# Kernel optimization log

Hardware: AMD Instinct MI355X
Metric: run time of the kernel (lower is better)

The kernel has to match this reference:

```python
import jax, jax.numpy as jnp
import numpy as np

B, L, D = 4, 2048, 1024
H, HD = 16, 64
SCALE = 1.0 / np.sqrt(H).astype(np.float32)  # NOTE: source divides by sqrt(head_num), not sqrt(head_dim)
NEG = -10000000.0


def setup_inputs() -> dict:
    key = jax.random.key(0)
    ks = jax.random.split(key, 7)
    s = 1.0 / np.sqrt(D).astype(np.float32)
    return {
        "X": jax.random.normal(ks[0], (B, L, D), dtype=jnp.float32),
        "Wq": jax.random.normal(ks[1], (D, D), dtype=jnp.float32) * s,
        "bq": jnp.zeros((D,), dtype=jnp.float32),
        "Wk": jax.random.normal(ks[2], (D, D), dtype=jnp.float32) * s,
        "bk": jnp.zeros((D,), dtype=jnp.float32),
        "Wv": jax.random.normal(ks[3], (D, D), dtype=jnp.float32) * s,
        "bv": jnp.zeros((D,), dtype=jnp.float32),
    }


def _split_heads(x):
    # [B, L, D] -> [B, H, L, HD]
    return x.reshape(B, L, H, HD).transpose(0, 2, 1, 3)


def reference(X, Wq, bq, Wk, bk, Wv, bv):
    Q = _split_heads(X @ Wq.T + bq)
    K = _split_heads(X @ Wk.T + bk)
    V = _split_heads(X @ Wv.T + bv)
    logits = jnp.einsum('bhld,bhmd->bhlm', Q, K) * SCALE
    # causal mask: strictly-upper-triangular entries get a large negative additive bias
    mask = jnp.triu(jnp.full((L, L), NEG, dtype=logits.dtype), k=1)
    logits = logits + mask[None, None, :, :]
    w = jax.nn.softmax(logits, axis=-1)
    out = jnp.einsum('bhlm,bhmd->bhld', w, V)
    # combine heads: [B, H, L, HD] -> [B, L, D]
    return out.transpose(0, 2, 1, 3).reshape(B, L, H * HD)
```

## Files before the change

### kernel.cpp

```cpp
#include <hip/hip_runtime.h>
#include <hip/hip_bf16.h>

#define L_SEQ   2048
#define DMODEL  1024
#define NH      16
#define HD      64
#define MROWS   8192
#define QSC     0.360673760222f
#define NEG2    -2.0e7f

typedef float  f32x4 __attribute__((ext_vector_type(4)));
typedef short  s16x8 __attribute__((ext_vector_type(8)));

__device__ __forceinline__ unsigned short f2bf(float f) {
    union { float f; unsigned u; } v; v.f = f;
    unsigned r = (v.u + 0x7FFFu + ((v.u >> 16) & 1u)) >> 16;
    return (unsigned short)r;
}

__device__ __forceinline__ float fexp2(float x) {
#if __has_builtin(__builtin_amdgcn_exp2f)
    return __builtin_amdgcn_exp2f(x);
#else
    return __expf(x * 0.6931471805599453f);
#endif
}

__device__ __forceinline__ unsigned pk2(float a, float b) {
    union { float f; unsigned u; } ua, ub; ua.f = a; ub.f = b;
    return __builtin_amdgcn_perm(ub.u, ua.u, 0x07060302u);
}

__device__ __forceinline__ void gl_lds16(const void* g, void* l) {
    __builtin_amdgcn_global_load_lds(
        (const __attribute__((address_space(1))) unsigned int*)g,
        (__attribute__((address_space(3))) unsigned int*)l, 16, 0, 0);
}

__global__ __launch_bounds__(256) void cvt_all(const float* __restrict__ X,
                                               const float* __restrict__ W0,
                                               const float* __restrict__ W1,
                                               const float* __restrict__ W2,
                                               unsigned short* __restrict__ Xb,
                                               unsigned short* __restrict__ Wb) {
    const int bx = blockIdx.x, tid = threadIdx.x;
    const float* src; unsigned short* dst; int i;
    if (bx < 8192) {
        src = X; dst = Xb; i = bx * 256 + tid;
    } else {
        int r = bx - 8192; const int wsel = r >> 10; r &= 1023;
        src = (wsel == 0) ? W0 : (wsel == 1) ? W1 : W2;
        dst = Wb + (size_t)wsel * (DMODEL * DMODEL);
        i = r * 256 + tid;
    }
    float4 v = ((const float4*)src)[i];
    ushort4 o;
    o.x = f2bf(v.x); o.y = f2bf(v.y); o.z = f2bf(v.z); o.w = f2bf(v.w);
    ((ushort4*)dst)[i] = o;
}

__global__ __launch_bounds__(256, 2) void qkv_gemm(
        const unsigned short* __restrict__ Xb,
        const unsigned short* __restrict__ Wb,
        const float* __restrict__ bq, const float* __restrict__ bk_,
        const float* __restrict__ bv,
        unsigned short* __restrict__ Yb) {
    __shared__ unsigned short As[128 * 32];
    __shared__ unsigned short Bs[128 * 32];

    const int tid = threadIdx.x;
    const int w = tid >> 6, l = tid & 63, q = l >> 4, t = l & 15;
    const int mw = w >> 1, nw = w & 1;
    const int z = blockIdx.z;
    const int rowM0 = blockIdx.x * 128;
    const int colN0 = blockIdx.y * 128;

    const unsigned short* W = Wb + (size_t)z * (DMODEL * DMODEL);
    unsigned short* Y = Yb + (size_t)z * ((size_t)MROWS * DMODEL);
    const float* bias = (z == 0) ? bq : (z == 1) ? bk_ : bv;
    const float osc = (z == 0) ? QSC : 1.0f;

    f32x4 acc[4][4] = {};

    const int srow = l >> 2;
    const int scol = (l & 3) * 8;

    for (int k0 = 0; k0 < DMODEL; k0 += 32) {
        #pragma unroll
        for (int r = 0; r < 2; ++r) {
            const int row = w * 32 + r * 16;
            gl_lds16(Xb + (size_t)(rowM0 + row + srow) * DMODEL + k0 + scol, As + row * 32);
            gl_lds16(W  + (size_t)(colN0 + row + srow) * DMODEL + k0 + scol, Bs + row * 32);
        }
        __syncthreads();
        s16x8 a[4], b[4];
        #pragma unroll
        for (int i = 0; i < 4; ++i) {
            a[i] = *(const s16x8*)&As[(mw * 64 + i * 16 + t) * 32 + q * 8];
            b[i] = *(const s16x8*)&Bs[(nw * 64 + i * 16 + t) * 32 + q * 8];
        }
        #pragma unroll
        for (int in = 0; in < 4; ++in)
            #pragma unroll
            for (int jm = 0; jm < 4; ++jm)
                acc[in][jm] = __builtin_amdgcn_mfma_f32_16x16x32_bf16(b[in], a[jm], acc[in][jm], 0, 0, 0);
        __syncthreads();
    }

    #pragma unroll
    for (int in = 0; in < 4; ++in) {
        const int ncol = colN0 + nw * 64 + in * 16 + q * 4;
        const float4 b4 = *(const float4*)&bias[ncol];
        #pragma unroll
        for (int jm = 0; jm < 4; ++jm) {
            const int mrow = rowM0 + mw * 64 + jm * 16 + t;
            unsigned lo = ((unsigned)f2bf((acc[in][jm][0] + b4.x) * osc)) |
                          ((unsigned)f2bf((acc[in][jm][1] + b4.y) * osc) << 16);
            unsigned hi = ((unsigned)f2bf((acc[in][jm][2] + b4.z) * osc)) |
                          ((unsigned)f2bf((acc[in][jm][3] + b4.w) * osc) << 16);
            uint2 o; o.x = lo; o.y = hi;
            *(uint2*)&Y[(size_t)mrow * DMODEL + ncol] = o;
        }
    }
}

#define SKV 72

__global__ __launch_bounds__(256, 4) void attn_fwd(
        const unsigned short* __restrict__ Qb,
        const unsigned short* __restrict__ Kb,
        const unsigned short* __restrict__ Vb,
        float* __restrict__ out) {
    __shared__ __align__(16) unsigned short Ks[2][64 * 64];
    __shared__ __align__(16) unsigned short Vt[2][64 * SKV];

    const int tid = threadIdx.x;
    const int w = tid >> 6, l = tid & 63, q = l >> 4, t = l & 15;

    const int lin = blockIdx.y * gridDim.x + blockIdx.x;
    const int xcd = lin & 7;
    const int slot = lin >> 3;
    const int bh = ((slot >> 4) << 3) | xcd;
    const int pairx = slot & 15;

    const int b = bh >> 4, h = bh & 15;
    const size_t base = ((size_t)b * L_SEQ) * DMODEL + h * HD;

    const int d8 = tid >> 5, jp = tid & 31;
    const int vslot = ((jp >> 4) << 5) | (((jp >> 1) & 3) << 3) | (((jp >> 3) & 1) << 2) | ((jp & 1) << 1);
    const int krow_in = l >> 3;
    const int kchunk_g = (l & 7) ^ krow_in;

    int kaddr[4][2];
    #pragma unroll
    for (int nt = 0; nt < 4; ++nt)
        #pragma unroll
        for (int ks = 0; ks < 2; ++ks)
            kaddr[nt][ks] = (nt * 16 + t) * 64 + (((ks * 4 + q) ^ (t & 7)) * 8);

    s16x8 vone;
    #pragma unroll
    for (int i = 0; i < 8; ++i) vone[i] = (short)0x3F80;

    auto stageK = [&](int jbase, unsigned short* dst) {
        #pragma unroll
        for (int r = 0; r < 2; ++r) {
            const int rb = r * 4 + w;
            gl_lds16(Kb + base + (size_t)(jbase + rb * 8 + krow_in) * DMODEL + kchunk_g * 8,
                     dst + rb * 512);
        }
    };
    auto stageV = [&](int jbase, unsigned short* dst) {
        const unsigned short* vp = Vb + base + (size_t)(jbase + 2 * jp) * DMODEL + d8 * 8;
        uint4 v0 = *(const uint4*)vp;
        uint4 v1 = *(const uint4*)(vp + DMODEL);
        const unsigned* u0 = (const unsigned*)&v0;
        const unsigned* u1 = (const unsigned*)&v1;
        #pragma unroll
        for (int i = 0; i < 4; ++i) {
            *(unsigned*)&dst[(d8 * 8 + 2 * i)     * SKV + vslot] = __builtin_amdgcn_perm(u1[i], u0[i], 0x05040100u);
            *(unsigned*)&dst[(d8 * 8 + 2 * i + 1) * SKV + vslot] = __builtin_amdgcn_perm(u1[i], u0[i], 0x07060302u);
        }
    };

    for (int pass = 0; pass < 2; ++pass) {
        const int qt = pass ? (31 - pairx) : pairx;
        const int qbase = qt * 64;

        s16x8 bq[2];
        {
            const unsigned short* qp = Qb + base + (size_t)(qbase + w * 16 + t) * DMODEL + q * 8;
            bq[0] = *(const s16x8*)(qp);
            bq[1] = *(const s16x8*)(qp + 32);
        }

        float m_i = -__builtin_inff();
        f32x4 accO[4] = {};
        f32x4 accL = {};

        auto loadS = [&](const unsigned short* KsBuf, f32x4* stt) {
            #pragma unroll
            for (int nt = 0; nt < 4; ++nt) {
                f32x4 zz = {};
                #pragma unroll
                for (int ks = 0; ks < 2; ++ks) {
                    s16x8 ak = *(const s16x8*)&KsBuf[kaddr[nt][ks]];
                    zz = __builtin_amdgcn_mfma_f32_16x16x32_bf16(ak, bq[ks], zz, 0, 0, 0);
                }
                stt[nt] = zz;
            }
        };
        auto maskS = [&](f32x4* stt) {
            const int rhs = w * 16 + t;
            #pragma unroll
            for (int nt = 0; nt < 4; ++nt)
                #pragma unroll
                for (int r = 0; r < 4; ++r)
                    if (nt * 16 + q * 4 + r > rhs) stt[nt][r] += NEG2;
        };
        auto rescale = [&](float m_new) {
            const float alpha = fexp2(m_i - m_new);
            m_i = m_new;
            float ar[4];
            #pragma unroll
            for (int r = 0; r < 4; ++r) ar[r] = __shfl(alpha, q * 4 + r, 64);
            #pragma unroll
            for (int nt = 0; nt < 4; ++nt)
                #pragma unroll
                for (int r = 0; r < 4; ++r) accO[nt][r] *= ar[r];
            #pragma unroll
            for (int r = 0; r < 4; ++r) accL[r] *= ar[r];
        };
        auto pvAcc = [&](const f32x4* stt, float m_new, const unsigned short* VtBuf) {
            union { unsigned u[8]; s16x8 h[2]; } P;
            #pragma unroll
            for (int nt = 0; nt < 4; ++nt) {
                float p0 = fexp2(stt[nt][0] - m_new);
                float p1 = fexp2(stt[nt][1] - m_new);
                float p2 = fexp2(stt[nt][2] - m_new);
                float p3 = fexp2(stt[nt][3] - m_new);
                P.u[2 * nt]     = pk2(p0, p1);
                P.u[2 * nt + 1] = pk2(p2, p3);
            }
            #pragma unroll
            for (int ks = 0; ks < 2; ++ks) {
                #pragma unroll
                for (int nt = 0; nt < 4; ++nt) {
                    s16x8 vb = *(const s16x8*)&VtBuf[(nt * 16 + t) * SKV + ks * 32 + q * 8];
                    accO[nt] = __builtin_amdgcn_mfma_f32_16x16x32_bf16(P.h[ks], vb, accO[nt], 0, 0, 0);
                }
                accL = __builtin_amdgcn_mfma_f32_16x16x32_bf16(P.h[ks], vone, accL, 0, 0, 0);
            }
        };

        int jt = 0;
        for (; jt + 1 <= qt; jt += 2) {
            __syncthreads();
            stageK(jt * 64, Ks[0]); stageK(jt * 64 + 64, Ks[1]);
            stageV(jt * 64, Vt[0]); stageV(jt * 64 + 64, Vt[1]);
            __syncthreads();

            f32x4 s0[4], s1[4];
            loadS(Ks[0], s0);
            loadS(Ks[1], s1);
            if (jt + 1 == qt) maskS(s1);

            float mx = s0[0][0];
            #pragma unroll
            for (int nt = 0; nt < 4; ++nt)
                #pragma unroll
                for (int r = 0; r < 4; ++r) { mx = fmaxf(mx, s0[nt][r]); mx = fmaxf(mx, s1[nt][r]); }
            mx = fmaxf(mx, __shfl_xor(mx, 16, 64));
            mx = fmaxf(mx, __shfl_xor(mx, 32, 64));
            const float m_new = fmaxf(m_i, mx);

            rescale(m_new);
            pvAcc(s0, m_new, Vt[0]);
            pvAcc(s1, m_new, Vt[1]);
        }
        if (jt == qt) {
            __syncthreads();
            stageK(qbase, Ks[0]);
            stageV(qbase, Vt[0]);
            __syncthreads();

            f32x4 s0[4];
            loadS(Ks[0], s0);
            maskS(s0);

            float mx = s0[0][0];
            #pragma unroll
            for (int nt = 0; nt < 4; ++nt)
                #pragma unroll
                for (int r = 0; r < 4; ++r) mx = fmaxf(mx, s0[nt][r]);
            mx = fmaxf(mx, __shfl_xor(mx, 16, 64));
            mx = fmaxf(mx, __shfl_xor(mx, 32, 64));
            const float m_new = fmaxf(m_i, mx);

            rescale(m_new);
            pvAcc(s0, m_new, Vt[0]);
        }

        float inv_r[4];
        #pragma unroll
        for (int r = 0; r < 4; ++r) inv_r[r] = 1.0f / accL[r];
        #pragma unroll
        for (int nt = 0; nt < 4; ++nt) {
            #pragma unroll
            for (int r = 0; r < 4; ++r) {
                const int row = qbase + w * 16 + q * 4 + r;
                out[((size_t)(b * L_SEQ + row)) * DMODEL + h * HD + nt * 16 + t] =
                    accO[nt][r] * inv_r[r];
            }
        }
    }
}

extern "C" void kernel_launch(void* const* d_in, const int* in_sizes, int n_in,
                              void* d_out, int out_size, void* d_ws, size_t ws_size,
                              hipStream_t stream) {
    const float* X  = (const float*)d_in[0];
    const float* Wq = (const float*)d_in[1];
    const float* bq = (const float*)d_in[2];
    const float* Wk = (const float*)d_in[3];
    const float* bk = (const float*)d_in[4];
    const float* Wv = (const float*)d_in[5];
    const float* bv = (const float*)d_in[6];
    float* out = (float*)d_out;

    unsigned short* Xb = (unsigned short*)d_ws;
    unsigned short* Wb = Xb + (size_t)MROWS * DMODEL;
    unsigned short* Yb = Wb + (size_t)3 * DMODEL * DMODEL;

    cvt_all<<<8192 + 3 * 1024, 256, 0, stream>>>(X, Wq, Wk, Wv, Xb, Wb);

    qkv_gemm<<<dim3(64, 8, 3), 256, 0, stream>>>(Xb, Wb, bq, bk, bv, Yb);

    const size_t hs = (size_t)MROWS * DMODEL;
    attn_fwd<<<dim3(16, 64), 256, 0, stream>>>(Yb, Yb + hs, Yb + 2 * hs, out);
}
```

Measured before the change: 229.7 us.

## Write QKV in head-major layout and widen GEMM K-tile with swizzled LDS

The QKV GEMM epilogue now writes Q/K/V in [B,H,L,HD] order, so the attention kernel reads contiguous 128-byte rows per head instead of strided rows across the full model dimension. The GEMM K-step doubles to 64 with an XOR-swizzled shared-memory layout, which halves the barrier count and aims to reduce LDS bank conflicts. This costs more LDS per block, which may reduce occupancy, and the epilogue's global stores are now scattered across heads.

```diff
diff --git a/kernel.cpp b/kernel.cpp
--- a/kernel.cpp
+++ b/kernel.cpp
@@ -65,8 +65,8 @@
         const float* __restrict__ bq, const float* __restrict__ bk_,
         const float* __restrict__ bv,
         unsigned short* __restrict__ Yb) {
-    __shared__ unsigned short As[128 * 32];
-    __shared__ unsigned short Bs[128 * 32];
+    __shared__ unsigned short As[128 * 64];
+    __shared__ unsigned short Bs[128 * 64];
 
     const int tid = threadIdx.x;
     const int w = tid >> 6, l = tid & 63, q = l >> 4, t = l & 15;
@@ -82,44 +82,54 @@
 
     f32x4 acc[4][4] = {};
 
-    const int srow = l >> 2;
-    const int scol = (l & 3) * 8;
-
-    for (int k0 = 0; k0 < DMODEL; k0 += 32) {
-        #pragma unroll
-        for (int r = 0; r < 2; ++r) {
-            const int row = w * 32 + r * 16;
-            gl_lds16(Xb + (size_t)(rowM0 + row + srow) * DMODEL + k0 + scol, As + row * 32);
-            gl_lds16(W  + (size_t)(colN0 + row + srow) * DMODEL + k0 + scol, Bs + row * 32);
+    const int srow8 = l >> 3;
+    const int sch_g = ((l & 7) ^ srow8) * 8;
+
+    const int coff0 = ((q) ^ (t & 7)) * 8;
+    const int coff1 = ((4 + q) ^ (t & 7)) * 8;
+
+    for (int k0 = 0; k0 < DMODEL; k0 += 64) {
+        #pragma unroll
+        for (int r = 0; r < 4; ++r) {
+            const int row = w * 32 + r * 8;
+            gl_lds16(Xb + (size_t)(rowM0 + row + srow8) * DMODEL + k0 + sch_g, As + row * 64);
+            gl_lds16(W  + (size_t)(colN0 + row + srow8) * DMODEL + k0 + sch_g, Bs + row * 64);
         }
         __syncthreads();
-        s16x8 a[4], b[4];
-        #pragma unroll
-        for (int i = 0; i < 4; ++i) {
-            a[i] = *(const s16x8*)&As[(mw * 64 + i * 16 + t) * 32 + q * 8];
-            b[i] = *(const s16x8*)&Bs[(nw * 64 + i * 16 + t) * 32 + q * 8];
-        }
-        #pragma unroll
-        for (int in = 0; in < 4; ++in)
-            #pragma unroll
-            for (int jm = 0; jm < 4; ++jm)
-                acc[in][jm] = __builtin_amdgcn_mfma_f32_16x16x32_bf16(b[in], a[jm], acc[in][jm], 0, 0, 0);
+        #pragma unroll
+        for (int ks = 0; ks < 2; ++ks) {
+            const int co = ks ? coff1 : coff0;
+            s16x8 a[4], b[4];
+            #pragma unroll
+            for (int i = 0; i < 4; ++i) {
+                a[i] = *(const s16x8*)&As[(mw * 64 + i * 16 + t) * 64 + co];
+                b[i] = *(const s16x8*)&Bs[(nw * 64 + i * 16 + t) * 64 + co];
+            }
+            #pragma unroll
+            for (int in = 0; in < 4; ++in)
+                #pragma unroll
+                for (int jm = 0; jm < 4; ++jm)
+                    acc[in][jm] = __builtin_amdgcn_mfma_f32_16x16x32_bf16(b[in], a[jm], acc[in][jm], 0, 0, 0);
+        }
         __syncthreads();
     }
 
+    const int bb = rowM0 >> 11;
     #pragma unroll
     for (int in = 0; in < 4; ++in) {
         const int ncol = colN0 + nw * 64 + in * 16 + q * 4;
+        const int hh = ncol >> 6, hd = ncol & 63;
         const float4 b4 = *(const float4*)&bias[ncol];
+        unsigned short* Yh = Y + ((size_t)(bb * NH + hh) * L_SEQ) * HD + hd;
         #pragma unroll
         for (int jm = 0; jm < 4; ++jm) {
-            const int mrow = rowM0 + mw * 64 + jm * 16 + t;
+            const int sl = (rowM0 & 2047) + mw * 64 + jm * 16 + t;
             unsigned lo = ((unsigned)f2bf((acc[in][jm][0] + b4.x) * osc)) |
                           ((unsigned)f2bf((acc[in][jm][1] + b4.y) * osc) << 16);
             unsigned hi = ((unsigned)f2bf((acc[in][jm][2] + b4.z) * osc)) |
                           ((unsigned)f2bf((acc[in][jm][3] + b4.w) * osc) << 16);
             uint2 o; o.x = lo; o.y = hi;
-            *(uint2*)&Y[(size_t)mrow * DMODEL + ncol] = o;
+            *(uint2*)&Yh[(size_t)sl * HD] = o;
         }
     }
 }
@@ -144,7 +154,7 @@
     const int pairx = slot & 15;
 
     const int b = bh >> 4, h = bh & 15;
-    const size_t base = ((size_t)b * L_SEQ) * DMODEL + h * HD;
+    const size_t base = (size_t)bh * (L_SEQ * HD);
 
     const int d8 = tid >> 5, jp = tid & 31;
     const int vslot = ((jp >> 4) << 5) | (((jp >> 1) & 3) << 3) | (((jp >> 3) & 1) << 2) | ((jp & 1) << 1);
@@ -166,14 +176,14 @@
         #pragma unroll
         for (int r = 0; r < 2; ++r) {
             const int rb = r * 4 + w;
-            gl_lds16(Kb + base + (size_t)(jbase + rb * 8 + krow_in) * DMODEL + kchunk_g * 8,
+            gl_lds16(Kb + base + (size_t)(jbase + rb * 8 + krow_in) * HD + kchunk_g * 8,
                      dst + rb * 512);
         }
     };
     auto stageV = [&](int jbase, unsigned short* dst) {
-        const unsigned short* vp = Vb + base + (size_t)(jbase + 2 * jp) * DMODEL + d8 * 8;
+        const unsigned short* vp = Vb + base + (size_t)(jbase + 2 * jp) * HD + d8 * 8;
         uint4 v0 = *(const uint4*)vp;
-        uint4 v1 = *(const uint4*)(vp + DMODEL);
+        uint4 v1 = *(const uint4*)(vp + HD);
         const unsigned* u0 = (const unsigned*)&v0;
         const unsigned* u1 = (const unsigned*)&v1;
         #pragma unroll
@@ -189,7 +199,7 @@
 
         s16x8 bq[2];
         {
-            const unsigned short* qp = Qb + base + (size_t)(qbase + w * 16 + t) * DMODEL + q * 8;
+            const unsigned short* qp = Qb + base + (size_t)(qbase + w * 16 + t) * HD + q * 8;
             bq[0] = *(const s16x8*)(qp);
             bq[1] = *(const s16x8*)(qp + 32);
         }
```

Result: faster. 213.1 us (-7.3%).
